# Optimization experiments

Hardware: AMD Instinct MI355X
Metric: run time of the kernel (lower is better)

## Reference

```python
import jax, jax.numpy as jnp
import numpy as np

B, S, F = 2048, 64, 16
H = 512
E = 8
HORIZON = 8
HH = H // 2


def _lstm_cell(x, h, c, Wih, Whh, b):
    # PyTorch gate order: i, f, g, o
    z = x @ Wih.T + h @ Whh.T + b  # [B, 4H]
    i, f, g, o = jnp.split(z, 4, axis=-1)
    c2 = jax.nn.sigmoid(f) * c + jax.nn.sigmoid(i) * jnp.tanh(g)
    h2 = jax.nn.sigmoid(o) * jnp.tanh(c2)
    return h2, c2


def _run_lstm(xs, Wih, Whh, b):
    # xs: [S, B, in]; returns outs [S, B, H], h_n, c_n
    Bv = xs.shape[1]
    h0 = jnp.zeros((Bv, H), xs.dtype)
    c0 = jnp.zeros((Bv, H), xs.dtype)

    def step(carry, xt):
        h, c = carry
        h, c = _lstm_cell(xt, h, c, Wih, Whh, b)
        return (h, c), h

    (h_n, c_n), outs = jax.lax.scan(step, (h0, c0), xs)
    return outs, h_n, c_n


def setup_inputs() -> dict:
    key = jax.random.key(0)
    ks = iter(jax.random.split(key, 40))
    s = 1.0 / np.sqrt(H)

    def rn(shape, scale=None):
        sc = s if scale is None else scale
        return (jax.random.normal(next(ks), shape, dtype=jnp.float32) * sc)

    inp = {
        'x': jax.random.normal(next(ks), (B, S, F), dtype=jnp.float32),
        # encoder LSTM layer 0 (in=F) and layer 1 (in=H); b = b_ih + b_hh fused
        'enc_Wih0': rn((4 * H, F)), 'enc_Whh0': rn((4 * H, H)), 'enc_b0': rn((4 * H,)),
        'enc_Wih1': rn((4 * H, H)), 'enc_Whh1': rn((4 * H, H)), 'enc_b1': rn((4 * H,)),
        # decoder LSTM (in=4)
        'dec_Wih': rn((4 * H, 4)), 'dec_Whh': rn((4 * H, H)), 'dec_b': rn((4 * H,)),
        # gating MLP
        'gW1': rn((HH, H)), 'gb1': rn((HH,)), 'gW2': rn((E, HH)), 'gb2': rn((E,)),
        # experts, stacked over E: track(2), intensity(1), wind_abs(1)
        'tW1': rn((E, HH, H)), 'tb1': rn((E, HH)), 'tW2': rn((E, 2, HH)), 'tb2': rn((E, 2)),
        'iW1': rn((E, HH, H)), 'ib1': rn((E, HH)), 'iW2': rn((E, 1, HH)), 'ib2': rn((E, 1)),
        'wW1': rn((E, HH, H)), 'wb1': rn((E, HH)), 'wW2': rn((E, 1, HH)), 'wb2': rn((E, 1)),
    }
    return inp


def _forward(x, enc_Wih0, enc_Whh0, enc_b0, enc_Wih1, enc_Whh1, enc_b1,
             dec_Wih, dec_Whh, dec_b, gW1, gb1, gW2, gb2,
             tW1, tb1, tW2, tb2, iW1, ib1, iW2, ib2, wW1, wb1, wW2, wb2):
    xs = jnp.swapaxes(x, 0, 1)  # [S, B, F]
    outs0, _, _ = _run_lstm(xs, enc_Wih0, enc_Whh0, enc_b0)
    _, h_n, c_n = _run_lstm(outs0, enc_Wih1, enc_Whh1, enc_b1)
    # (attention-pooled context of encoder is computed then discarded in the
    #  original forward; it does not affect outputs, so it is omitted here)

    dec_in0 = jnp.zeros((x.shape[0], 4), x.dtype)

    def step(carry, _):
        h, c, dec_in = carry
        h, c = _lstm_cell(dec_in, h, c, dec_Wih, dec_Whh, dec_b)
        ctx = h  # [B, H]
        gates = jax.nn.softmax(jax.nn.relu(ctx @ gW1.T + gb1) @ gW2.T + gb2, axis=-1)  # [B, E]
        def expert(W1, b1, W2, b2):
            hdd = jax.nn.relu(jnp.einsum('ehd,bd->beh', W1, ctx) + b1)  # [B, E, HH]
            return jnp.einsum('eoh,beh->beo', W2, hdd) + b2  # [B, E, out]
        track_e = expert(tW1, tb1, tW2, tb2)   # [B, E, 2]
        dwind_e = expert(iW1, ib1, iW2, ib2)   # [B, E, 1]
        wind_e = expert(wW1, wb1, wW2, wb2)    # [B, E, 1]
        g = gates[:, :, None]
        track = (g * track_e).sum(1)  # [B, 2]
        dwind = (g * dwind_e).sum(1)  # [B, 1]
        wind = (g * wind_e).sum(1)    # [B, 1]
        dec_in2 = jnp.concatenate([track, dwind, wind], axis=-1)  # [B, 4]
        return (h, c, dec_in2), (track, dwind[:, 0], wind[:, 0], gates)

    _, (trk, dw, wa, gt) = jax.lax.scan(step, (h_n, c_n, dec_in0), None, length=HORIZON)
    # trk: [T, B, 2]; dw, wa: [T, B]; gt: [T, B, E]
    dlat = trk[:, :, 0].T  # [B, T]
    dlon = trk[:, :, 1].T
    track = jnp.concatenate([dlat, dlon], axis=1)  # [B, 2T]
    intensity = dw.T  # [B, T]
    wind_abs = wa.T   # [B, T]
    gates_avg = gt.mean(0)  # [B, E]
    return track, intensity, wind_abs, gates_avg


def reference(x, enc_Wih0, enc_Whh0, enc_b0, enc_Wih1, enc_Whh1, enc_b1,
              dec_Wih, dec_Whh, dec_b, gW1, gb1, gW2, gb2,
              tW1, tb1, tW2, tb2, iW1, ib1, iW2, ib2, wW1, wb1, wW2, wb2):
    return _forward(x, enc_Wih0, enc_Whh0, enc_b0, enc_Wih1, enc_Whh1, enc_b1,
                    dec_Wih, dec_Whh, dec_b, gW1, gb1, gW2, gb2,
                    tW1, tb1, tW2, tb2, iW1, ib1, iW2, ib2, wW1, wb1, wW2, wb2)
```

## Files before the change

kernel.cpp:

```cpp
#include <hip/hip_runtime.h>
#include <math.h>

#define B_SZ 2048
#define SEQ 64
#define H 512
#define G4 2048
#define HH 256
#define NE 8
#define HOR 8

typedef _Float16 v8h __attribute__((ext_vector_type(8)));
typedef _Float16 v4h __attribute__((ext_vector_type(4)));
typedef float v4f __attribute__((ext_vector_type(4)));

__device__ __forceinline__ void gld16(const void* g, void* l) {
    __builtin_amdgcn_global_load_lds((const __attribute__((address_space(1))) void*)g,
                                     (__attribute__((address_space(3))) void*)l, 16, 0, 0);
}
__device__ __forceinline__ v4f mfma16(v8h a, v8h b, v4f c) {
    return __builtin_amdgcn_mfma_f32_16x16x32_f16(a, b, c, 0, 0, 0);
}
__device__ __forceinline__ float rcp_(float x) { return __builtin_amdgcn_rcpf(x); }
__device__ __forceinline__ float sigf(float x) { return rcp_(1.f + __expf(-x)); }
__device__ __forceinline__ float tanhf_(float x) { return 1.f - 2.f * rcp_(1.f + __expf(2.f * x)); }


struct CellP {
    const _Float16* Af; int KTA;
    const _Float16* Bf;
    const float* bias; int KT;
    float* cst;
    _Float16* h1p; int h1kt, h1o;
    _Float16* h2p; int h2kt, h2o;
    const _Float16* xsrc; _Float16* xdst;
};

__global__ __launch_bounds__(256, 4)
void cell2_k(CellP P0, CellP P1, int zbase)
{
    __shared__ __align__(16) char smem[34816];
    const CellP& P = (blockIdx.z + zbase == 0) ? P0 : P1;
    _Float16* st = (_Float16*)smem;
    float* zb = (float*)smem;
    const int tid = threadIdx.x, lane = tid & 63, wv = tid >> 6;
    const int bx = blockIdx.x, by = blockIdx.y;
    const int KT = P.KT;

    const _Float16* pA0 = P.Af + ((long)(by * 8 + 2 * wv) * P.KTA) * 512 + lane * 8;
    const _Float16* pA1 = P.Af + ((long)(by * 8 + 2 * wv + 1) * P.KTA) * 512 + lane * 8;
    const _Float16* pB0 = P.Bf + ((long)(bx * 8 + 2 * wv) * KT) * 512 + lane * 8;
    const _Float16* pB1 = P.Bf + ((long)(bx * 8 + 2 * wv + 1) * KT) * 512 + lane * 8;
    const int oA0 = 2 * wv * 512, oA1 = oA0 + 512;
    const int oB0 = 4096 + 2 * wv * 512, oB1 = oB0 + 512;
    const int wm = (wv & 1) * 64, wn = (wv >> 1) * 64;
    const int fr = lane & 15, q4 = (lane >> 4) * 4;

    v4f acc[4][4];
    #pragma unroll
    for (int i = 0; i < 4; i++)
        #pragma unroll
        for (int j = 0; j < 4; j++) acc[i][j] = (v4f){0.f, 0.f, 0.f, 0.f};

    gld16(pA0, st + oA0); gld16(pA1, st + oA1);
    gld16(pB0, st + oB0); gld16(pB1, st + oB1);
    pA0 += 512; pA1 += 512; pB0 += 512; pB1 += 512;

    for (int kt = 0; kt < KT; ++kt) {
        __syncthreads();
        const int cur = kt & 1;
        if (kt + 1 < KT) {
            _Float16* nb = st + (cur ^ 1) * 8192;
            gld16(pA0, nb + oA0); gld16(pA1, nb + oA1);
            gld16(pB0, nb + oB0); gld16(pB1, nb + oB1);
            pA0 += 512; pA1 += 512; pB0 += 512; pB1 += 512;
        }
        const _Float16* base = st + cur * 8192;
        v8h bf[4];
        #pragma unroll
        for (int nt = 0; nt < 4; ++nt)
            bf[nt] = *(const v8h*)(base + 4096 + ((wv >> 1) * 4 + nt) * 512 + lane * 8);
        #pragma unroll
        for (int mt = 0; mt < 4; ++mt) {
            v8h a = *(const v8h*)(base + ((wv & 1) * 4 + mt) * 512 + lane * 8);
            #pragma unroll
            for (int nt = 0; nt < 4; ++nt)
                acc[mt][nt] = mfma16(a, bf[nt], acc[mt][nt]);
        }
    }

    #pragma unroll
    for (int half = 0; half < 2; ++half) {
        __syncthreads();
        if ((wv >> 1) == half) {
            #pragma unroll
            for (int mt = 0; mt < 4; ++mt)
                #pragma unroll
                for (int nt = 0; nt < 4; ++nt) {
                    int col = nt * 16 + fr;
                    float bv = P.bias[bx * 128 + half * 64 + col];
                    #pragma unroll
                    for (int r = 0; r < 4; ++r)
                        zb[(wm + mt * 16 + q4 + r) * 68 + col] = acc[mt][nt][r] + bv;
                }
        }
        __syncthreads();
        const int row = tid >> 1, u8 = (tid & 1) * 8;
        const long b = by * 128 + row;
        const int ug = bx * 32 + half * 16 + u8;
        float* cp = P.cst + b * 512 + ug;
        float4 cl0 = *(float4*)cp, cl1 = *(float4*)(cp + 4);
        float cv[8] = {cl0.x, cl0.y, cl0.z, cl0.w, cl1.x, cl1.y, cl1.z, cl1.w};
        v8h hv;
        #pragma unroll
        for (int i = 0; i < 8; ++i) {
            const float* zz = &zb[row * 68 + (u8 + i) * 4];
            float cn = sigf(zz[1]) * cv[i] + sigf(zz[0]) * tanhf_(zz[2]);
            cv[i] = cn;
            hv[i] = (_Float16)(sigf(zz[3]) * tanhf_(cn));
        }
        *(float4*)cp = make_float4(cv[0], cv[1], cv[2], cv[3]);
        *(float4*)(cp + 4) = make_float4(cv[4], cv[5], cv[6], cv[7]);
        {
            int kk = P.h1o + ug;
            long a = ((b >> 4) * (long)P.h1kt + (kk >> 5)) * 512 + (((kk & 31) >> 3) * 16 + (b & 15)) * 8;
            *(v8h*)(P.h1p + a) = hv;
        }
        if (P.h2p) {
            int kk = P.h2o + ug;
            long a = ((b >> 4) * (long)P.h2kt + (kk >> 5)) * 512 + (((kk & 31) >> 3) * 16 + (b & 15)) * 8;
            *(v8h*)(P.h2p + a) = hv;
        }
        if (half == 0 && P.xsrc != nullptr && bx == 0) {
            int mc = tid >> 5, l = tid & 31;
            v8h xv = *(const v8h*)(P.xsrc + ((long)(by * 8 + mc) * 32 + l) * 8);
            *(v8h*)(P.xdst + (((long)(by * 8 + mc)) * 17 + 16) * 512 + l * 8) = xv;
        }
    }
}

__global__ __launch_bounds__(256, 4)
void expert_k(const _Float16* __restrict__ Af, const _Float16* __restrict__ W1f,
              const float* __restrict__ b1, const float* __restrict__ w2all,
              float* __restrict__ pe, _Float16* __restrict__ t1)
{
    __shared__ __align__(16) char smem[32768];
    _Float16* st = (_Float16*)smem;
    float* red = (float*)smem;
    const int tid = threadIdx.x, lane = tid & 63, wv = tid >> 6;
    const int bx = blockIdx.x, by = blockIdx.y;
    const long z = blockIdx.z;

    const _Float16* pA0 = Af + ((long)(by * 8 + 2 * wv) * 17) * 512 + lane * 8;
    const _Float16* pA1 = Af + ((long)(by * 8 + 2 * wv + 1) * 17) * 512 + lane * 8;
    const _Float16* pB0 = W1f + ((z * 16 + bx * 8 + 2 * wv) * 16) * 512 + lane * 8;
    const _Float16* pB1 = W1f + ((z * 16 + bx * 8 + 2 * wv + 1) * 16) * 512 + lane * 8;
    const int oA0 = 2 * wv * 512, oA1 = oA0 + 512;
    const int oB0 = 4096 + 2 * wv * 512, oB1 = oB0 + 512;
    const int wm = (wv & 1) * 64, wn = (wv >> 1) * 64;
    const int fr = lane & 15, q4 = (lane >> 4) * 4;

    v4f acc[4][4];
    #pragma unroll
    for (int i = 0; i < 4; i++)
        #pragma unroll
        for (int j = 0; j < 4; j++) acc[i][j] = (v4f){0.f, 0.f, 0.f, 0.f};

    gld16(pA0, st + oA0); gld16(pA1, st + oA1);
    gld16(pB0, st + oB0); gld16(pB1, st + oB1);
    pA0 += 512; pA1 += 512; pB0 += 512; pB1 += 512;

    for (int kt = 0; kt < 16; ++kt) {
        __syncthreads();
        const int cur = kt & 1;
        if (kt + 1 < 16) {
            _Float16* nb = st + (cur ^ 1) * 8192;
            gld16(pA0, nb + oA0); gld16(pA1, nb + oA1);
            gld16(pB0, nb + oB0); gld16(pB1, nb + oB1);
            pA0 += 512; pA1 += 512; pB0 += 512; pB1 += 512;
        }
        const _Float16* base = st + cur * 8192;
        v8h bf[4];
        #pragma unroll
        for (int nt = 0; nt < 4; ++nt)
            bf[nt] = *(const v8h*)(base + 4096 + ((wv >> 1) * 4 + nt) * 512 + lane * 8);
        #pragma unroll
        for (int mt = 0; mt < 4; ++mt) {
            v8h a = *(const v8h*)(base + ((wv & 1) * 4 + mt) * 512 + lane * 8);
            #pragma unroll
            for (int nt = 0; nt < 4; ++nt)
                acc[mt][nt] = mfma16(a, bf[nt], acc[mt][nt]);
        }
    }
    __syncthreads();

    if (z == 24) {
        #pragma unroll
        for (int mt = 0; mt < 4; ++mt)
            #pragma unroll
            for (int nt = 0; nt < 4; ++nt) {
                int col = bx * 128 + wn + nt * 16 + fr;
                float bv = b1[24 * 256 + col];
                #pragma unroll
                for (int r = 0; r < 4; ++r) {
                    float v = fmaxf(acc[mt][nt][r] + bv, 0.f);
                    t1[(long)(by * 128 + wm + mt * 16 + q4 + r) * 256 + col] = (_Float16)v;
                }
            }
        return;
    }
    float w0[4], w1[4], bv[4];
    #pragma unroll
    for (int nt = 0; nt < 4; ++nt) {
        int col = bx * 128 + wn + nt * 16 + fr;
        w0[nt] = w2all[(z * 2 + 0) * 256 + col];
        w1[nt] = w2all[(z * 2 + 1) * 256 + col];
        bv[nt] = b1[z * 256 + col];
    }
    float p0[4][4], p1[4][4];
    #pragma unroll
    for (int mt = 0; mt < 4; ++mt)
        #pragma unroll
        for (int r = 0; r < 4; ++r) { p0[mt][r] = 0.f; p1[mt][r] = 0.f; }
    #pragma unroll
    for (int mt = 0; mt < 4; ++mt)
        #pragma unroll
        for (int nt = 0; nt < 4; ++nt)
            #pragma unroll
            for (int r = 0; r < 4; ++r) {
                float v = fmaxf(acc[mt][nt][r] + bv[nt], 0.f);
                p0[mt][r] = fmaf(v, w0[nt], p0[mt][r]);
                p1[mt][r] = fmaf(v, w1[nt], p1[mt][r]);
            }
    #pragma unroll
    for (int off = 1; off < 16; off <<= 1)
        #pragma unroll
        for (int mt = 0; mt < 4; ++mt)
            #pragma unroll
            for (int r = 0; r < 4; ++r) {
                p0[mt][r] += __shfl_xor(p0[mt][r], off, 64);
                p1[mt][r] += __shfl_xor(p1[mt][r], off, 64);
            }
    if ((lane & 15) == 0) {
        #pragma unroll
        for (int mt = 0; mt < 4; ++mt)
            #pragma unroll
            for (int r = 0; r < 4; ++r) {
                int row = wm + mt * 16 + q4 + r;
                red[(((wv >> 1) * 128) + row) * 2 + 0] = p0[mt][r];
                red[(((wv >> 1) * 128) + row) * 2 + 1] = p1[mt][r];
            }
    }
    __syncthreads();
    if (tid < 128) {
        #pragma unroll
        for (int o = 0; o < 2; ++o) {
            float v = red[tid * 2 + o] + red[(128 + tid) * 2 + o];
            pe[(((long)bx * 24 + z) * 2 + o) * 2048 + by * 128 + tid] = v;
        }
    }
}

__global__ __launch_bounds__(256)
void fin_k(const _Float16* __restrict__ t1, const float* __restrict__ gW2,
           const float* __restrict__ gb2, const float* __restrict__ pe,
           const float* __restrict__ tb2, const float* __restrict__ ib2,
           const float* __restrict__ wb2,
           float* __restrict__ out, _Float16* __restrict__ dw, int step)
{
    const long b = blockIdx.x * 256 + threadIdx.x;
    float acc[NE];
    #pragma unroll
    for (int e = 0; e < NE; e++) acc[e] = gb2[e];
    for (int j = 0; j < 256; j += 8) {
        v8h tv = *(const v8h*)(t1 + b * 256 + j);
        #pragma unroll
        for (int k = 0; k < 8; ++k) {
            float xv = (float)tv[k];
            #pragma unroll
            for (int e = 0; e < NE; e++) acc[e] = fmaf(xv, gW2[e * 256 + j + k], acc[e]);
        }
    }
    float mx = -1e30f;
    #pragma unroll
    for (int e = 0; e < NE; e++) mx = fmaxf(mx, acc[e]);
    float s = 0.f;
    #pragma unroll
    for (int e = 0; e < NE; e++) { acc[e] = __expf(acc[e] - mx); s += acc[e]; }
    float inv = 1.f / s;
    float t0 = 0.f, t1v = 0.f, iv = 0.f, wvv = 0.f;
    #pragma unroll
    for (int e = 0; e < NE; e++) {
        float g = acc[e] * inv;
        float prev = step == 0 ? 0.f : out[32 * (long)B_SZ + b * NE + e];
        out[32 * (long)B_SZ + b * NE + e] = prev + g * (1.f / HOR);
        float s00 = pe[((0 * 24 + e) * 2 + 0) * 2048 + b] + pe[((1 * 24 + e) * 2 + 0) * 2048 + b];
        float s01 = pe[((0 * 24 + e) * 2 + 1) * 2048 + b] + pe[((1 * 24 + e) * 2 + 1) * 2048 + b];
        float s10 = pe[((0 * 24 + 8 + e) * 2 + 0) * 2048 + b] + pe[((1 * 24 + 8 + e) * 2 + 0) * 2048 + b];
        float s20 = pe[((0 * 24 + 16 + e) * 2 + 0) * 2048 + b] + pe[((1 * 24 + 16 + e) * 2 + 0) * 2048 + b];
        t0  += g * (s00 + tb2[e * 2 + 0]);
        t1v += g * (s01 + tb2[e * 2 + 1]);
        iv  += g * (s10 + ib2[e]);
        wvv += g * (s20 + wb2[e]);
    }
    out[b * 16 + step] = t0;
    out[b * 16 + 8 + step] = t1v;
    out[16 * (long)B_SZ + b * 8 + step] = iv;
    out[24 * (long)B_SZ + b * 8 + step] = wvv;
    v4h dv = {(_Float16)t0, (_Float16)t1v, (_Float16)iv, (_Float16)wvv};
    *(v4h*)(dw + ((b >> 4) * 17 + 16) * 512 + (b & 15) * 8) = dv;
}

__global__ __launch_bounds__(64)
void prep_wfrag(const float* __restrict__ s1, int K1, const float* __restrict__ s2, int K2,
                _Float16* __restrict__ dst, int KT,
                const float* __restrict__ bs, float* __restrict__ bd)
{
    const int nc = blockIdx.x, kt = blockIdx.y, l = threadIdx.x;
    const int nprime = nc * 16 + (l & 15);
    const int u = nprime >> 2, g = nprime & 3, srow = g * 512 + u;
    v8h v;
    #pragma unroll
    for (int j = 0; j < 8; ++j) {
        int k = kt * 32 + (l >> 4) * 8 + j;
        float val = 0.f;
        if (k < K1) val = s1[(long)srow * K1 + k];
        else if (k < K1 + K2) val = s2[(long)srow * K2 + k - K1];
        v[j] = (_Float16)val;
    }
    *(v8h*)(dst + ((long)nc * KT + kt) * 512 + l * 8) = v;
    if (kt == 0 && l < 16) bd[nc * 16 + l] = bs[((nc * 16 + l) & 3) * 512 + ((nc * 16 + l) >> 2)];
}

__global__ __launch_bounds__(64)
void prep_w1frag(const float* __restrict__ tW1, const float* __restrict__ iW1,
                 const float* __restrict__ wW1, const float* __restrict__ gW1,
                 _Float16* __restrict__ dst)
{
    const int nc = blockIdx.x & 15, kt = blockIdx.x >> 4, z = blockIdx.y, l = threadIdx.x;
    const float* src;
    if (z < 8) src = tW1 + (long)z * 256 * 512;
    else if (z < 16) src = iW1 + (long)(z - 8) * 256 * 512;
    else if (z < 24) src = wW1 + (long)(z - 16) * 256 * 512;
    else src = gW1;
    const int row = nc * 16 + (l & 15);
    v8h v;
    #pragma unroll
    for (int j = 0; j < 8; ++j)
        v[j] = (_Float16)src[(long)row * 512 + kt * 32 + (l >> 4) * 8 + j];
    *(v8h*)(dst + (((long)z * 16 + nc) * 16 + kt) * 512 + l * 8) = v;
}

__global__ __launch_bounds__(256)
void cat4(const float* __restrict__ a, const float* __restrict__ b,
          const float* __restrict__ c, const float* __restrict__ g,
          float* __restrict__ d)
{
    int i = blockIdx.x * 256 + threadIdx.x;
    float v;
    if (i < 2048) v = a[i];
    else if (i < 4096) v = b[i - 2048];
    else if (i < 6144) v = c[i - 4096];
    else v = g[i - 6144];
    d[i] = v;
}

__global__ __launch_bounds__(256)
void prep_w2(const float* __restrict__ tW2, const float* __restrict__ iW2,
             const float* __restrict__ wW2, float* __restrict__ W2all)
{
    int i = blockIdx.x * 256 + threadIdx.x;
    int j = i & 255, o = (i >> 8) & 1, zz = i >> 9;
    int br = zz >> 3, e = zz & 7;
    float v = 0.f;
    if (br == 0) v = tW2[(e * 2 + o) * 256 + j];
    else if (o == 0) v = (br == 1 ? iW2 : wW2)[e * 256 + j];
    W2all[i] = v;
}

__global__ __launch_bounds__(256)
void prep_xf(const float* __restrict__ x, _Float16* __restrict__ xTf,
             _Float16* __restrict__ act0a)
{
    const int t = blockIdx.x * 256 + threadIdx.x;
    const int l = t & 31, mc = (t >> 5) & 127, s = t >> 12;
    const long b = mc * 16 + (l & 15);
    const float* src = x + (b * 64 + s) * 16 + (l >> 4) * 8;
    v8h v;
    #pragma unroll
    for (int j = 0; j < 8; ++j) v[j] = (_Float16)src[j];
    *(v8h*)(xTf + (((long)s * 128 + mc) * 32 + l) * 8) = v;
    if (s == 0) *(v8h*)(act0a + ((long)mc * 17 + 16) * 512 + l * 8) = v;
}

extern "C" void kernel_launch(void* const* d_in, const int* in_sizes, int n_in,
                              void* d_out, int out_size, void* d_ws, size_t ws_size,
                              hipStream_t stream)
{
    const float* x    = (const float*)d_in[0];
    const float* Wih0 = (const float*)d_in[1];
    const float* Whh0 = (const float*)d_in[2];
    const float* b0   = (const float*)d_in[3];
    const float* Wih1 = (const float*)d_in[4];
    const float* Whh1 = (const float*)d_in[5];
    const float* b1   = (const float*)d_in[6];
    const float* dWih = (const float*)d_in[7];
    const float* dWhh = (const float*)d_in[8];
    const float* db   = (const float*)d_in[9];
    const float* gW1  = (const float*)d_in[10];
    const float* gb1  = (const float*)d_in[11];
    const float* gW2  = (const float*)d_in[12];
    const float* gb2  = (const float*)d_in[13];
    const float* tW1  = (const float*)d_in[14];
    const float* tb1  = (const float*)d_in[15];
    const float* tW2  = (const float*)d_in[16];
    const float* tb2  = (const float*)d_in[17];
    const float* iW1  = (const float*)d_in[18];
    const float* ib1  = (const float*)d_in[19];
    const float* iW2  = (const float*)d_in[20];
    const float* ib2  = (const float*)d_in[21];
    const float* wW1  = (const float*)d_in[22];
    const float* wb1  = (const float*)d_in[23];
    const float* wW2  = (const float*)d_in[24];
    const float* wb2  = (const float*)d_in[25];
    float* out = (float*)d_out;

    char* p = (char*)d_ws;
    auto alloc = [&](size_t bytes) { char* r = p; p += (bytes + 255) & ~255ULL; return r; };
    _Float16* xTf   = (_Float16*)alloc((size_t)SEQ * 128 * 32 * 8 * 2);
    _Float16* act0a = (_Float16*)alloc((size_t)128 * 17 * 512 * 2);
    _Float16* act0b = (_Float16*)alloc((size_t)128 * 17 * 512 * 2);
    _Float16* act1a = (_Float16*)alloc((size_t)128 * 32 * 512 * 2);
    _Float16* act1b = (_Float16*)alloc((size_t)128 * 32 * 512 * 2);
    _Float16* actDa = (_Float16*)alloc((size_t)128 * 17 * 512 * 2);
    _Float16* actDb = (_Float16*)alloc((size_t)128 * 17 * 512 * 2);
    float*    c0    = (float*)alloc((size_t)B_SZ * 512 * 4);
    float*    c1    = (float*)alloc((size_t)B_SZ * 512 * 4);
    _Float16* Wc0   = (_Float16*)alloc((size_t)128 * 17 * 512 * 2);
    _Float16* Wc1   = (_Float16*)alloc((size_t)128 * 32 * 512 * 2);
    _Float16* Wcd   = (_Float16*)alloc((size_t)128 * 17 * 512 * 2);
    float*    b0i   = (float*)alloc((size_t)G4 * 4);
    float*    b1i   = (float*)alloc((size_t)G4 * 4);
    float*    bdi   = (float*)alloc((size_t)G4 * 4);
    _Float16* W1all = (_Float16*)alloc((size_t)25 * 16 * 16 * 512 * 2);
    float*    b1all = (float*)alloc((size_t)25 * HH * 4);
    float*    W2all = (float*)alloc((size_t)24 * 2 * 256 * 4);
    _Float16* t1    = (_Float16*)alloc((size_t)B_SZ * HH * 2);
    float*    pe    = (float*)alloc((size_t)2 * 24 * 2 * 2048 * 4);

    hipMemsetAsync(act0a, 0, (size_t)128 * 17 * 512 * 2, stream);
    hipMemsetAsync(act0b, 0, (size_t)128 * 17 * 512 * 2, stream);
    hipMemsetAsync(act1a, 0, (size_t)128 * 32 * 512 * 2, stream);
    hipMemsetAsync(act1b, 0, (size_t)128 * 32 * 512 * 2, stream);
    hipMemsetAsync(actDa, 0, (size_t)128 * 17 * 512 * 2, stream);
    hipMemsetAsync(actDb, 0, (size_t)128 * 17 * 512 * 2, stream);
    hipMemsetAsync(c0, 0, (size_t)B_SZ * 512 * 4, stream);
    hipMemsetAsync(c1, 0, (size_t)B_SZ * 512 * 4, stream);

    prep_wfrag<<<dim3(128, 17), dim3(64), 0, stream>>>(Whh0, 512, Wih0, 16, Wc0, 17, b0, b0i);
    prep_wfrag<<<dim3(128, 32), dim3(64), 0, stream>>>(Wih1, 512, Whh1, 512, Wc1, 32, b1, b1i);
    prep_wfrag<<<dim3(128, 17), dim3(64), 0, stream>>>(dWhh, 512, dWih, 4, Wcd, 17, db, bdi);
    prep_w1frag<<<dim3(256, 25), dim3(64), 0, stream>>>(tW1, iW1, wW1, gW1, W1all);
    cat4<<<dim3(25), dim3(256), 0, stream>>>(tb1, ib1, wb1, gb1, b1all);
    prep_w2<<<dim3(48), dim3(256), 0, stream>>>(tW2, iW2, wW2, W2all);
    prep_xf<<<dim3(1024), dim3(256), 0, stream>>>(x, xTf, act0a);

    _Float16* act0[2] = {act0a, act0b};
    _Float16* act1[2] = {act1a, act1b};

    for (int s = 0; s <= SEQ; ++s) {
        const bool do0 = (s < SEQ), do1 = (s >= 1);
        CellP P0 = {}, P1 = {};
        if (do0) {
            P0.Af = act0[s & 1]; P0.KTA = 17;
            P0.Bf = Wc0; P0.bias = b0i; P0.KT = 17;
            P0.cst = c0;
            P0.h1p = act0[(s + 1) & 1]; P0.h1kt = 17; P0.h1o = 0;
            P0.h2p = act1[s & 1]; P0.h2kt = 32; P0.h2o = 0;
            P0.xsrc = (s < SEQ - 1) ? (xTf + ((long)(s + 1) * 128 * 32) * 8) : nullptr;
            P0.xdst = act0[(s + 1) & 1];
        }
        if (do1) {
            P1.Af = act1[(s + 1) & 1]; P1.KTA = 32;
            P1.Bf = Wc1; P1.bias = b1i; P1.KT = 32;
            P1.cst = c1;
            P1.h1p = act1[s & 1]; P1.h1kt = 32; P1.h1o = 512;
            P1.h2p = (s == SEQ) ? actDa : nullptr; P1.h2kt = 17; P1.h2o = 0;
            P1.xsrc = nullptr; P1.xdst = nullptr;
        }
        const int nz = (do0 && do1) ? 2 : 1;
        const int zbase = do0 ? 0 : 1;
        cell2_k<<<dim3(16, 16, nz), dim3(256), 0, stream>>>(P0, P1, zbase);
    }

    for (int t = 0; t < HOR; ++t) {
        _Float16* dr = (t & 1) ? actDb : actDa;
        _Float16* dw = (t & 1) ? actDa : actDb;
        CellP PD = {};
        PD.Af = dr; PD.KTA = 17;
        PD.Bf = Wcd; PD.bias = bdi; PD.KT = 17;
        PD.cst = c1;
        PD.h1p = dw; PD.h1kt = 17; PD.h1o = 0;
        PD.h2p = nullptr; PD.xsrc = nullptr; PD.xdst = nullptr;
        cell2_k<<<dim3(16, 16, 1), dim3(256), 0, stream>>>(PD, PD, 0);
        expert_k<<<dim3(2, 16, 25), dim3(256), 0, stream>>>(dw, W1all, b1all, W2all, pe, t1);
        fin_k<<<dim3(8), dim3(256), 0, stream>>>(t1, gW2, gb2, pe, tb2, ib2, wb2, out, dw, t);
    }
}
```

Before: 2.073 ms.

## Double K-step per LDS stage in LSTM cell GEMM, pad K tiles to even count

The cell GEMM now stages two 32-wide K tiles per iteration into 64KB of shared memory, which halves the number of barrier and prefetch rounds. Launch bounds drop to 2 blocks per CU to fit the larger buffers. To get an even tile count, the layer-0 and decoder activation and weight fragment buffers are padded from 17 to 18 K tiles, and every producer and consumer is updated to match. The padded tile adds some redundant MFMA work on zeros, and the larger shared-memory footprint lowers occupancy.

```diff
diff --git a/kernel.cpp b/kernel.cpp
--- a/kernel.cpp
+++ b/kernel.cpp
@@ -35,24 +35,24 @@
     const _Float16* xsrc; _Float16* xdst;
 };
 
-__global__ __launch_bounds__(256, 4)
+__global__ __launch_bounds__(256, 2)
 void cell2_k(CellP P0, CellP P1, int zbase)
 {
-    __shared__ __align__(16) char smem[34816];
+    __shared__ __align__(16) char smem[65536];
     const CellP& P = (blockIdx.z + zbase == 0) ? P0 : P1;
     _Float16* st = (_Float16*)smem;
     float* zb = (float*)smem;
     const int tid = threadIdx.x, lane = tid & 63, wv = tid >> 6;
     const int bx = blockIdx.x, by = blockIdx.y;
-    const int KT = P.KT;
+    const int NIT = P.KT >> 1;
 
     const _Float16* pA0 = P.Af + ((long)(by * 8 + 2 * wv) * P.KTA) * 512 + lane * 8;
     const _Float16* pA1 = P.Af + ((long)(by * 8 + 2 * wv + 1) * P.KTA) * 512 + lane * 8;
-    const _Float16* pB0 = P.Bf + ((long)(bx * 8 + 2 * wv) * KT) * 512 + lane * 8;
-    const _Float16* pB1 = P.Bf + ((long)(bx * 8 + 2 * wv + 1) * KT) * 512 + lane * 8;
-    const int oA0 = 2 * wv * 512, oA1 = oA0 + 512;
-    const int oB0 = 4096 + 2 * wv * 512, oB1 = oB0 + 512;
-    const int wm = (wv & 1) * 64, wn = (wv >> 1) * 64;
+    const _Float16* pB0 = P.Bf + ((long)(bx * 8 + 2 * wv) * P.KT) * 512 + lane * 8;
+    const _Float16* pB1 = P.Bf + ((long)(bx * 8 + 2 * wv + 1) * P.KT) * 512 + lane * 8;
+    const int oA = 4 * wv * 512;
+    const int oB = 8192 + 4 * wv * 512;
+    const int wm = (wv & 1) * 64;
     const int fr = lane & 15, q4 = (lane >> 4) * 4;
 
     v4f acc[4][4];
@@ -61,30 +61,37 @@
         #pragma unroll
         for (int j = 0; j < 4; j++) acc[i][j] = (v4f){0.f, 0.f, 0.f, 0.f};
 
-    gld16(pA0, st + oA0); gld16(pA1, st + oA1);
-    gld16(pB0, st + oB0); gld16(pB1, st + oB1);
-    pA0 += 512; pA1 += 512; pB0 += 512; pB1 += 512;
-
-    for (int kt = 0; kt < KT; ++kt) {
+    auto stage = [&](int buf, int it) {
+        _Float16* d = st + buf * 16384;
+        const long ko = (long)it * 1024;
+        gld16(pA0 + ko,       d + oA);
+        gld16(pA0 + ko + 512, d + oA + 512);
+        gld16(pA1 + ko,       d + oA + 1024);
+        gld16(pA1 + ko + 512, d + oA + 1536);
+        gld16(pB0 + ko,       d + oB);
+        gld16(pB0 + ko + 512, d + oB + 512);
+        gld16(pB1 + ko,       d + oB + 1024);
+        gld16(pB1 + ko + 512, d + oB + 1536);
+    };
+
+    stage(0, 0);
+    for (int it = 0; it < NIT; ++it) {
         __syncthreads();
-        const int cur = kt & 1;
-        if (kt + 1 < KT) {
-            _Float16* nb = st + (cur ^ 1) * 8192;
-            gld16(pA0, nb + oA0); gld16(pA1, nb + oA1);
-            gld16(pB0, nb + oB0); gld16(pB1, nb + oB1);
-            pA0 += 512; pA1 += 512; pB0 += 512; pB1 += 512;
-        }
-        const _Float16* base = st + cur * 8192;
-        v8h bf[4];
-        #pragma unroll
-        for (int nt = 0; nt < 4; ++nt)
-            bf[nt] = *(const v8h*)(base + 4096 + ((wv >> 1) * 4 + nt) * 512 + lane * 8);
-        #pragma unroll
-        for (int mt = 0; mt < 4; ++mt) {
-            v8h a = *(const v8h*)(base + ((wv & 1) * 4 + mt) * 512 + lane * 8);
+        if (it + 1 < NIT) stage((it & 1) ^ 1, it + 1);
+        const _Float16* base = st + (it & 1) * 16384;
+        #pragma unroll
+        for (int p = 0; p < 2; ++p) {
+            v8h bf[4];
             #pragma unroll
             for (int nt = 0; nt < 4; ++nt)
-                acc[mt][nt] = mfma16(a, bf[nt], acc[mt][nt]);
+                bf[nt] = *(const v8h*)(base + 8192 + (((wv >> 1) * 4 + nt) * 2 + p) * 512 + lane * 8);
+            #pragma unroll
+            for (int mt = 0; mt < 4; ++mt) {
+                v8h a = *(const v8h*)(base + (((wv & 1) * 4 + mt) * 2 + p) * 512 + lane * 8);
+                #pragma unroll
+                for (int nt = 0; nt < 4; ++nt)
+                    acc[mt][nt] = mfma16(a, bf[nt], acc[mt][nt]);
+            }
         }
     }
 
@@ -133,7 +140,7 @@
         if (half == 0 && P.xsrc != nullptr && bx == 0) {
             int mc = tid >> 5, l = tid & 31;
             v8h xv = *(const v8h*)(P.xsrc + ((long)(by * 8 + mc) * 32 + l) * 8);
-            *(v8h*)(P.xdst + (((long)(by * 8 + mc)) * 17 + 16) * 512 + l * 8) = xv;
+            *(v8h*)(P.xdst + (((long)(by * 8 + mc)) * 18 + 16) * 512 + l * 8) = xv;
         }
     }
 }
@@ -150,8 +157,8 @@
     const int bx = blockIdx.x, by = blockIdx.y;
     const long z = blockIdx.z;
 
-    const _Float16* pA0 = Af + ((long)(by * 8 + 2 * wv) * 17) * 512 + lane * 8;
-    const _Float16* pA1 = Af + ((long)(by * 8 + 2 * wv + 1) * 17) * 512 + lane * 8;
+    const _Float16* pA0 = Af + ((long)(by * 8 + 2 * wv) * 18) * 512 + lane * 8;
+    const _Float16* pA1 = Af + ((long)(by * 8 + 2 * wv + 1) * 18) * 512 + lane * 8;
     const _Float16* pB0 = W1f + ((z * 16 + bx * 8 + 2 * wv) * 16) * 512 + lane * 8;
     const _Float16* pB1 = W1f + ((z * 16 + bx * 8 + 2 * wv + 1) * 16) * 512 + lane * 8;
     const int oA0 = 2 * wv * 512, oA1 = oA0 + 512;
@@ -245,9 +252,9 @@
         for (int mt = 0; mt < 4; ++mt)
             #pragma unroll
             for (int r = 0; r < 4; ++r) {
-                int row = wm + mt * 16 + q4 + r;
-                red[(((wv >> 1) * 128) + row) * 2 + 0] = p0[mt][r];
-                red[(((wv >> 1) * 128) + row) * 2 + 1] = p1[mt][r];
+                int rw = wm + mt * 16 + q4 + r;
+                red[(((wv >> 1) * 128) + rw) * 2 + 0] = p0[mt][r];
+                red[(((wv >> 1) * 128) + rw) * 2 + 1] = p1[mt][r];
             }
     }
     __syncthreads();
@@ -307,7 +314,7 @@
     out[16 * (long)B_SZ + b * 8 + step] = iv;
     out[24 * (long)B_SZ + b * 8 + step] = wvv;
     v4h dv = {(_Float16)t0, (_Float16)t1v, (_Float16)iv, (_Float16)wvv};
-    *(v4h*)(dw + ((b >> 4) * 17 + 16) * 512 + (b & 15) * 8) = dv;
+    *(v4h*)(dw + ((b >> 4) * 18 + 16) * 512 + (b & 15) * 8) = dv;
 }
 
 __global__ __launch_bounds__(64)
@@ -389,7 +396,7 @@
     #pragma unroll
     for (int j = 0; j < 8; ++j) v[j] = (_Float16)src[j];
     *(v8h*)(xTf + (((long)s * 128 + mc) * 32 + l) * 8) = v;
-    if (s == 0) *(v8h*)(act0a + ((long)mc * 17 + 16) * 512 + l * 8) = v;
+    if (s == 0) *(v8h*)(act0a + ((long)mc * 18 + 16) * 512 + l * 8) = v;
 }
 
 extern "C" void kernel_launch(void* const* d_in, const int* in_sizes, int n_in,
@@ -427,17 +434,17 @@
     char* p = (char*)d_ws;
     auto alloc = [&](size_t bytes) { char* r = p; p += (bytes + 255) & ~255ULL; return r; };
     _Float16* xTf   = (_Float16*)alloc((size_t)SEQ * 128 * 32 * 8 * 2);
-    _Float16* act0a = (_Float16*)alloc((size_t)128 * 17 * 512 * 2);
-    _Float16* act0b = (_Float16*)alloc((size_t)128 * 17 * 512 * 2);
+    _Float16* act0a = (_Float16*)alloc((size_t)128 * 18 * 512 * 2);
+    _Float16* act0b = (_Float16*)alloc((size_t)128 * 18 * 512 * 2);
     _Float16* act1a = (_Float16*)alloc((size_t)128 * 32 * 512 * 2);
     _Float16* act1b = (_Float16*)alloc((size_t)128 * 32 * 512 * 2);
-    _Float16* actDa = (_Float16*)alloc((size_t)128 * 17 * 512 * 2);
-    _Float16* actDb = (_Float16*)alloc((size_t)128 * 17 * 512 * 2);
+    _Float16* actDa = (_Float16*)alloc((size_t)128 * 18 * 512 * 2);
+    _Float16* actDb = (_Float16*)alloc((size_t)128 * 18 * 512 * 2);
     float*    c0    = (float*)alloc((size_t)B_SZ * 512 * 4);
     float*    c1    = (float*)alloc((size_t)B_SZ * 512 * 4);
-    _Float16* Wc0   = (_Float16*)alloc((size_t)128 * 17 * 512 * 2);
+    _Float16* Wc0   = (_Float16*)alloc((size_t)128 * 18 * 512 * 2);
     _Float16* Wc1   = (_Float16*)alloc((size_t)128 * 32 * 512 * 2);
-    _Float16* Wcd   = (_Float16*)alloc((size_t)128 * 17 * 512 * 2);
+    _Float16* Wcd   = (_Float16*)alloc((size_t)128 * 18 * 512 * 2);
     float*    b0i   = (float*)alloc((size_t)G4 * 4);
     float*    b1i   = (float*)alloc((size_t)G4 * 4);
     float*    bdi   = (float*)alloc((size_t)G4 * 4);
@@ -447,18 +454,18 @@
     _Float16* t1    = (_Float16*)alloc((size_t)B_SZ * HH * 2);
     float*    pe    = (float*)alloc((size_t)2 * 24 * 2 * 2048 * 4);
 
-    hipMemsetAsync(act0a, 0, (size_t)128 * 17 * 512 * 2, stream);
-    hipMemsetAsync(act0b, 0, (size_t)128 * 17 * 512 * 2, stream);
+    hipMemsetAsync(act0a, 0, (size_t)128 * 18 * 512 * 2, stream);
+    hipMemsetAsync(act0b, 0, (size_t)128 * 18 * 512 * 2, stream);
     hipMemsetAsync(act1a, 0, (size_t)128 * 32 * 512 * 2, stream);
     hipMemsetAsync(act1b, 0, (size_t)128 * 32 * 512 * 2, stream);
-    hipMemsetAsync(actDa, 0, (size_t)128 * 17 * 512 * 2, stream);
-    hipMemsetAsync(actDb, 0, (size_t)128 * 17 * 512 * 2, stream);
+    hipMemsetAsync(actDa, 0, (size_t)128 * 18 * 512 * 2, stream);
+    hipMemsetAsync(actDb, 0, (size_t)128 * 18 * 512 * 2, stream);
     hipMemsetAsync(c0, 0, (size_t)B_SZ * 512 * 4, stream);
     hipMemsetAsync(c1, 0, (size_t)B_SZ * 512 * 4, stream);
 
-    prep_wfrag<<<dim3(128, 17), dim3(64), 0, stream>>>(Whh0, 512, Wih0, 16, Wc0, 17, b0, b0i);
+    prep_wfrag<<<dim3(128, 18), dim3(64), 0, stream>>>(Whh0, 512, Wih0, 16, Wc0, 18, b0, b0i);
     prep_wfrag<<<dim3(128, 32), dim3(64), 0, stream>>>(Wih1, 512, Whh1, 512, Wc1, 32, b1, b1i);
-    prep_wfrag<<<dim3(128, 17), dim3(64), 0, stream>>>(dWhh, 512, dWih, 4, Wcd, 17, db, bdi);
+    prep_wfrag<<<dim3(128, 18), dim3(64), 0, stream>>>(dWhh, 512, dWih, 4, Wcd, 18, db, bdi);
     prep_w1frag<<<dim3(256, 25), dim3(64), 0, stream>>>(tW1, iW1, wW1, gW1, W1all);
     cat4<<<dim3(25), dim3(256), 0, stream>>>(tb1, ib1, wb1, gb1, b1all);
     prep_w2<<<dim3(48), dim3(256), 0, stream>>>(tW2, iW2, wW2, W2all);
@@ -471,10 +478,10 @@
         const bool do0 = (s < SEQ), do1 = (s >= 1);
         CellP P0 = {}, P1 = {};
         if (do0) {
-            P0.Af = act0[s & 1]; P0.KTA = 17;
-            P0.Bf = Wc0; P0.bias = b0i; P0.KT = 17;
+            P0.Af = act0[s & 1]; P0.KTA = 18;
+            P0.Bf = Wc0; P0.bias = b0i; P0.KT = 18;
             P0.cst = c0;
-            P0.h1p = act0[(s + 1) & 1]; P0.h1kt = 17; P0.h1o = 0;
+            P0.h1p = act0[(s + 1) & 1]; P0.h1kt = 18; P0.h1o = 0;
             P0.h2p = act1[s & 1]; P0.h2kt = 32; P0.h2o = 0;
             P0.xsrc = (s < SEQ - 1) ? (xTf + ((long)(s + 1) * 128 * 32) * 8) : nullptr;
             P0.xdst = act0[(s + 1) & 1];
@@ -484,7 +491,7 @@
             P1.Bf = Wc1; P1.bias = b1i; P1.KT = 32;
             P1.cst = c1;
             P1.h1p = act1[s & 1]; P1.h1kt = 32; P1.h1o = 512;
-            P1.h2p = (s == SEQ) ? actDa : nullptr; P1.h2kt = 17; P1.h2o = 0;
+            P1.h2p = (s == SEQ) ? actDa : nullptr; P1.h2kt = 18; P1.h2o = 0;
             P1.xsrc = nullptr; P1.xdst = nullptr;
         }
         const int nz = (do0 && do1) ? 2 : 1;
@@ -496,10 +503,10 @@
         _Float16* dr = (t & 1) ? actDb : actDa;
         _Float16* dw = (t & 1) ? actDa : actDb;
         CellP PD = {};
-        PD.Af = dr; PD.KTA = 17;
-        PD.Bf = Wcd; PD.bias = bdi; PD.KT = 17;
+        PD.Af = dr; PD.KTA = 18;
+        PD.Bf = Wcd; PD.bias = bdi; PD.KT = 18;
         PD.cst = c1;
-        PD.h1p = dw; PD.h1kt = 17; PD.h1o = 0;
+        PD.h1p = dw; PD.h1kt = 18; PD.h1o = 0;
         PD.h2p = nullptr; PD.xsrc = nullptr; PD.xdst = nullptr;
         cell2_k<<<dim3(16, 16, 1), dim3(256), 0, stream>>>(PD, PD, 0);
         expert_k<<<dim3(2, 16, 25), dim3(256), 0, stream>>>(dw, W1all, b1all, W2all, pe, t1);
```

After: 1.952 ms, median of 2. 5.8% less time.
